# Kernel tuning notes

Hardware: AMD Instinct MI355X
Metric: run time of the kernel (lower is better)

Reference implementation:

```python
import jax, jax.numpy as jnp
import numpy as np

SMU_ALPHA = 0.25
SMU_MU = 1.0e6  # repo's act.SMU default: large mu -> smooth leaky-relu (max(x, alpha*x))

def smu(x):
    a = SMU_ALPHA
    return 0.5 * ((1.0 + a) * x + (1.0 - a) * x * jax.lax.erf(SMU_MU * (1.0 - a) * x))

def setup_inputs() -> dict:
    key = jax.random.key(0)
    ks = jax.random.split(key, 6)
    B, N, D = 8, 4096, 1024
    xavier = float(np.sqrt(6.0 / (D + D)))
    def lin_w(k):
        return jax.random.uniform(k, (D, D), jnp.float32, -xavier, xavier)
    return {
        "x": jax.random.normal(ks[0], (B, N, D), jnp.float32),
        "Wvr": lin_w(ks[1]), "bvr": jnp.zeros((D,), jnp.float32),
        "Wvi": lin_w(ks[2]), "bvi": jnp.zeros((D,), jnp.float32),
        "Wk": lin_w(ks[3]), "bk": jnp.zeros((D,), jnp.float32),
        "Wq": lin_w(ks[4]), "bq": jnp.zeros((D,), jnp.float32),
    }

def reference(x, Wvr, bvr, Wvi, bvi, Wk, bk, Wq, bq):
    # real input: real and imag branches both see x
    value_real = jnp.einsum('bnd,ed->bne', x, Wvr) + bvr
    value_imag = jnp.einsum('bnd,ed->bne', x, Wvi) + bvi
    # GLU: v_real * tanh(softplus(v_imag)); dropout disabled (p=0)
    value = value_real * jnp.tanh(jax.nn.softplus(value_imag))
    key_ = jnp.einsum('bnd,ed->bne', x, Wk) + bk
    query = jnp.einsum('bnd,ed->bne', x, Wq) + bq
    # L2 normalize along the sequence dim (dim=1)
    key_n = key_ / (jnp.linalg.norm(key_, axis=1, keepdims=True) + 1e-5)
    query_n = query / (jnp.linalg.norm(query, axis=1, keepdims=True) + 1e-5)
    feature_attn = smu(jnp.einsum('bnd,bne->bde', key_n, query_n))  # [B, D, D]
    return jnp.einsum('bnd,bde->bne', value, feature_attn)
```

## Files before the change

kernel.cpp:

```cpp
#include <hip/hip_runtime.h>
#include <math.h>

typedef __bf16 bf16x8 __attribute__((ext_vector_type(8)));
typedef float f32x4 __attribute__((ext_vector_type(4)));

#define MTOT 32768
#define DD   1024
#define NSEQ 4096
#define BB   8

__device__ __forceinline__ void async16(const void* gp, void* lp) {
  __builtin_amdgcn_global_load_lds(
      (__attribute__((address_space(1))) void*)(const_cast<void*>(gp)),
      (__attribute__((address_space(3))) void*)(lp), 16, 0, 0);
}

__device__ __forceinline__ unsigned short f2bf(float f) {
  union { float f; unsigned int u; } v; v.f = f;
  unsigned int r = v.u + 0x7fffu + ((v.u >> 16) & 1u);
  return (unsigned short)(r >> 16);
}
__device__ __forceinline__ float bf2f(unsigned short u) {
  union { unsigned int u; float f; } v; v.u = ((unsigned int)u) << 16; return v.f;
}

__device__ __forceinline__ unsigned lds_off(void* p) {
  return (unsigned)(unsigned long long)
      (__attribute__((address_space(3))) void*)p;
}
__device__ __forceinline__ bf16x8 dsr128(unsigned a) {
  bf16x8 r;
  asm volatile("ds_read_b128 %0, %1" : "=v"(r) : "v"(a));
  return r;
}

__global__ void cvt_bf16(const float* __restrict__ in, unsigned short* __restrict__ out, int n) {
  int i = (blockIdx.x * blockDim.x + threadIdx.x) * 8;
  if (i >= n) return;
  float4 a = *(const float4*)(in + i);
  float4 b = *(const float4*)(in + i + 4);
  ushort4 o0, o1;
  o0.x = f2bf(a.x); o0.y = f2bf(a.y); o0.z = f2bf(a.z); o0.w = f2bf(a.w);
  o1.x = f2bf(b.x); o1.y = f2bf(b.y); o1.z = f2bf(b.z); o1.w = f2bf(b.w);
  *(ushort4*)(out + i) = o0;
  *(ushort4*)(out + i + 4) = o1;
}

__global__ void cvt_w(const float* __restrict__ w0, const float* __restrict__ w1,
                      const float* __restrict__ w2, const float* __restrict__ w3,
                      unsigned short* __restrict__ out) {
  int z = blockIdx.y;
  const float* in = (z == 0) ? w0 : (z == 1) ? w1 : (z == 2) ? w2 : w3;
  int i = (blockIdx.x * blockDim.x + threadIdx.x) * 8;
  float4 a = *(const float4*)(in + i);
  float4 b = *(const float4*)(in + i + 4);
  ushort4 o0, o1;
  o0.x = f2bf(a.x); o0.y = f2bf(a.y); o0.z = f2bf(a.z); o0.w = f2bf(a.w);
  o1.x = f2bf(b.x); o1.y = f2bf(b.y); o1.z = f2bf(b.z); o1.w = f2bf(b.w);
  unsigned short* o = out + (size_t)z * DD * DD;
  *(ushort4*)(o + i) = o0;
  *(ushort4*)(o + i + 4) = o1;
}

template<int LDG>
__device__ __forceinline__ void stage_half(const unsigned short* __restrict__ g,
                                           int row0, int k0,
                                           unsigned short* lds, int tid) {
#pragma unroll
  for (int l = 0; l < 2; ++l) {
    int u = l * 512 + tid;
    int r = u >> 3;
    int sl = (u & 7) ^ (r & 7);
    async16(g + (size_t)(row0 + r) * LDG + k0 + sl * 8, (char*)lds + u * 16);
  }
}

__global__ __launch_bounds__(512, 2) void proj_all(
    const unsigned short* __restrict__ xb,
    const unsigned short* __restrict__ Wb,
    const float* __restrict__ bvr, const float* __restrict__ bvi,
    const float* __restrict__ bk,  const float* __restrict__ bq,
    unsigned short* __restrict__ oVr, unsigned short* __restrict__ oVi,
    unsigned short* __restrict__ Kt,  unsigned short* __restrict__ Qt,
    float* __restrict__ rnacc) {
  __shared__ __align__(16) unsigned short smem[65536];

  const int bx = blockIdx.x;
  const int swz = (bx & 7) * 64 + (bx >> 3);
  const int m0 = (swz >> 2) * 256;
  const int n0 = (swz & 3) * 256;
  const int z = blockIdx.z;
  const unsigned short* W = Wb + (size_t)z * DD * DD;
  const float* bias = (z == 0) ? bvr : (z == 1) ? bvi : (z == 2) ? bk : bq;

  const int tid = threadIdx.x;
  const int w = tid >> 6, lane = tid & 63;
  const int wr = w >> 2, wc = w & 3;
  const int lq = lane >> 4, lr = lane & 15;
  const int sx = lr & 7;
  const int arow0 = wr * 128 + lr;
  const int brow0 = wc * 64 + lr;

  f32x4 acc[8][4];
#pragma unroll
  for (int i = 0; i < 8; i++)
#pragma unroll
    for (int j = 0; j < 4; j++) acc[i][j] = (f32x4)(0.f);

  const int NT = 16;

  const unsigned sbase = lds_off(smem);
  const unsigned sw0 = (unsigned)((lq ^ sx) << 4);
  const unsigned sw1 = (unsigned)(((4 | lq) ^ sx) << 4);
  unsigned aA0 = sbase + arow0 * 128 + sw0;
  unsigned aA1 = sbase + arow0 * 128 + sw1;
  unsigned aB0 = sbase + 32768 + brow0 * 128 + sw0;
  unsigned aB1 = sbase + 32768 + brow0 * 128 + sw1;

  stage_half<1024>(xb, m0,       0,  smem,                     tid);
  stage_half<1024>(xb, m0 + 128, 0,  smem + 8192,              tid);
  stage_half<1024>(W,  n0,       0,  smem + 16384,             tid);
  stage_half<1024>(W,  n0 + 128, 0,  smem + 16384 + 8192,      tid);
  stage_half<1024>(W,  n0,       64, smem + 32768 + 16384,     tid);
  stage_half<1024>(W,  n0 + 128, 64, smem + 32768 + 16384 + 8192, tid);
  asm volatile("s_waitcnt vmcnt(4)" ::: "memory");
  __builtin_amdgcn_s_barrier();

  for (int t = 0; t < NT; ++t) {
    bf16x8 bfr[4][2];
#pragma unroll
    for (int q = 0; q < 4; ++q) {
      bf16x8 afq[2][2];
      if (q == 0) {
#pragma unroll
        for (int nj = 0; nj < 4; ++nj) {
          bfr[nj][0] = dsr128(aB0 + nj * 2048u);
          bfr[nj][1] = dsr128(aB1 + nj * 2048u);
        }
      }
#pragma unroll
      for (int mi = 0; mi < 2; ++mi) {
        afq[mi][0] = dsr128(aA0 + (2 * q + mi) * 2048u);
        afq[mi][1] = dsr128(aA1 + (2 * q + mi) * 2048u);
      }
      if (q == 0) {
        if (t + 1 < NT)
          stage_half<1024>(xb, m0, (t + 1) * 64, smem + ((t + 1) & 1) * 32768, tid);
      } else if (q == 1) {
        if (t + 1 < NT)
          stage_half<1024>(xb, m0 + 128, (t + 1) * 64, smem + ((t + 1) & 1) * 32768 + 8192, tid);
      } else if (q == 2) {
        if (t + 2 < NT)
          stage_half<1024>(W, n0, (t + 2) * 64, smem + (t & 1) * 32768 + 16384, tid);
      } else {
        if (t + 2 < NT)
          stage_half<1024>(W, n0 + 128, (t + 2) * 64, smem + (t & 1) * 32768 + 16384 + 8192, tid);
      }
      __builtin_amdgcn_s_barrier();
      asm volatile("s_waitcnt lgkmcnt(0)" ::: "memory");
      __builtin_amdgcn_sched_barrier(0);
      __builtin_amdgcn_s_setprio(1);
#pragma unroll
      for (int mi = 0; mi < 2; ++mi)
#pragma unroll
        for (int nj = 0; nj < 4; ++nj)
#pragma unroll
          for (int ks = 0; ks < 2; ++ks)
            acc[2 * q + mi][nj] = __builtin_amdgcn_mfma_f32_16x16x32_bf16(
                afq[mi][ks], bfr[nj][ks], acc[2 * q + mi][nj], 0, 0, 0);
      __builtin_amdgcn_s_setprio(0);
      __builtin_amdgcn_sched_barrier(0);
      if (q == 3) {
        if (t < NT - 2)       asm volatile("s_waitcnt vmcnt(4)" ::: "memory");
        else if (t == NT - 2) asm volatile("s_waitcnt vmcnt(0)" ::: "memory");
      }
      __builtin_amdgcn_s_barrier();
    }
    aA0 ^= 65536u; aA1 ^= 65536u; aB0 ^= 65536u; aB1 ^= 65536u;
  }

  if (z < 2) {
    unsigned short* out = (z == 0) ? oVr : oVi;
#pragma unroll
    for (int nj = 0; nj < 4; ++nj) {
      int col = n0 + wc * 64 + nj * 16 + lr;
      float bv = bias[col];
#pragma unroll
      for (int mrep = 0; mrep < 8; ++mrep) {
        int rowb = m0 + wr * 128 + mrep * 16 + lq * 4;
#pragma unroll
        for (int r = 0; r < 4; ++r)
          out[(size_t)(rowb + r) * DD + col] = f2bf(acc[mrep][nj][r] + bv);
      }
    }
  } else {
    unsigned short* outp = (z == 2) ? Kt : Qt;
    const int which = z - 2;
    const int b = m0 >> 12;
    const int nbase = m0 & 4095;
    float* racc = rnacc + which * (BB * DD) + b * DD;
    unsigned short* T = smem;
    const int SP2 = 264;
#pragma unroll
    for (int ch = 0; ch < 2; ++ch) {
      if ((wc >> 1) == ch) {
#pragma unroll
        for (int nj = 0; nj < 4; ++nj) {
          int cloc = (wc & 1) * 64 + nj * 16 + lr;
          float bv = bias[n0 + ch * 128 + cloc];
#pragma unroll
          for (int mrep = 0; mrep < 8; ++mrep) {
            int rowb = wr * 128 + mrep * 16 + lq * 4;
            ushort4 pk;
            pk.x = f2bf(acc[mrep][nj][0] + bv); pk.y = f2bf(acc[mrep][nj][1] + bv);
            pk.z = f2bf(acc[mrep][nj][2] + bv); pk.w = f2bf(acc[mrep][nj][3] + bv);
            *(ushort4*)(T + cloc * SP2 + rowb) = pk;
          }
        }
      }
      __syncthreads();
#pragma unroll
      for (int p = 0; p < 8; ++p) {
        int dl = p * 16 + (tid >> 5);
        int nc = (tid & 31) * 8;
        ushort4 v0 = *(const ushort4*)(T + dl * SP2 + nc);
        ushort4 v1 = *(const ushort4*)(T + dl * SP2 + nc + 4);
        int d = n0 + ch * 128 + dl;
        *(ushort4*)(outp + (size_t)(b * DD + d) * NSEQ + nbase + nc)     = v0;
        *(ushort4*)(outp + (size_t)(b * DD + d) * NSEQ + nbase + nc + 4) = v1;
        float s = bf2f(v0.x)*bf2f(v0.x) + bf2f(v0.y)*bf2f(v0.y) + bf2f(v0.z)*bf2f(v0.z) + bf2f(v0.w)*bf2f(v0.w)
                + bf2f(v1.x)*bf2f(v1.x) + bf2f(v1.y)*bf2f(v1.y) + bf2f(v1.z)*bf2f(v1.z) + bf2f(v1.w)*bf2f(v1.w);
#pragma unroll
        for (int off = 1; off < 32; off <<= 1) s += __shfl_xor(s, off, 32);
        if ((tid & 31) == 0) atomicAdd(&racc[d], s);
      }
      __syncthreads();
    }
  }
}

__global__ void finalize_rn(float* __restrict__ rn) {
  int i = blockIdx.x * blockDim.x + threadIdx.x;
  rn[i] = 1.f / (sqrtf(rn[i]) + 1e-5f);
}

__global__ void glu(unsigned short* __restrict__ V, const unsigned short* __restrict__ Vi, int n) {
  int i = (blockIdx.x * blockDim.x + threadIdx.x) * 8;
  if (i >= n) return;
  ushort4 r0 = *(const ushort4*)(V + i);
  ushort4 r1 = *(const ushort4*)(V + i + 4);
  ushort4 i0 = *(const ushort4*)(Vi + i);
  ushort4 i1 = *(const ushort4*)(Vi + i + 4);
  unsigned short vr[8] = {r0.x, r0.y, r0.z, r0.w, r1.x, r1.y, r1.z, r1.w};
  unsigned short vi[8] = {i0.x, i0.y, i0.z, i0.w, i1.x, i1.y, i1.z, i1.w};
  unsigned short o[8];
#pragma unroll
  for (int k = 0; k < 8; k++) {
    float a = bf2f(vr[k]), b = bf2f(vi[k]);
    float g;
    if (b > 10.f) g = 1.f;
    else { float t = __expf(b); float u = t * (t + 2.f); g = u / (u + 2.f); }
    o[k] = f2bf(a * g);
  }
  *(ushort4*)(V + i)     = make_ushort4(o[0], o[1], o[2], o[3]);
  *(ushort4*)(V + i + 4) = make_ushort4(o[4], o[5], o[6], o[7]);
}

__global__ __launch_bounds__(512, 2) void attn_gemm(
    const unsigned short* __restrict__ Qt, const unsigned short* __restrict__ Kt,
    const float* __restrict__ rn, unsigned short* __restrict__ fat) {
  __shared__ __align__(16) unsigned short smem[57344];

  const int b = blockIdx.z;
  const int d0 = blockIdx.x * 128;
  const int e0 = blockIdx.y * 256;
  const unsigned short* A  = Qt + (size_t)b * DD * NSEQ;
  const unsigned short* Bm = Kt + (size_t)b * DD * NSEQ;
  unsigned short* out = fat + (size_t)b * DD * DD;

  const int tid = threadIdx.x;
  const int w = tid >> 6, lane = tid & 63;
  const int wr = w >> 1, wc = w & 1;
  const int lq = lane >> 4, lr = lane & 15;
  const int sx = lr & 7;
  const int arow0 = wr * 64 + lr;
  const int brow0 = wc * 64 + lr;

  f32x4 acc[4][4];
#pragma unroll
  for (int i = 0; i < 4; i++)
#pragma unroll
    for (int j = 0; j < 4; j++) acc[i][j] = (f32x4)(0.f);

  const int NT = 64;

  const unsigned sbase = lds_off(smem);
  const unsigned sw0 = (unsigned)((lq ^ sx) << 4);
  const unsigned sw1 = (unsigned)(((4 | lq) ^ sx) << 4);
  unsigned aA0 = sbase + arow0 * 128 + sw0;
  unsigned aA1 = sbase + arow0 * 128 + sw1;
  unsigned aB0 = sbase + 32768 + brow0 * 128 + sw0;
  unsigned aB1 = sbase + 32768 + brow0 * 128 + sw1;

  stage_half<NSEQ>(A,  e0,       0,  smem,                 tid);
  stage_half<NSEQ>(A,  e0 + 128, 0,  smem + 8192,          tid);
  stage_half<NSEQ>(Bm, d0,       0,  smem + 16384,         tid);
  stage_half<NSEQ>(Bm, d0,       64, smem + 32768 + 16384, tid);
  asm volatile("s_waitcnt vmcnt(2)" ::: "memory");
  __builtin_amdgcn_s_barrier();

  for (int t = 0; t < NT; ++t) {
    bf16x8 bfr[4][2];
#pragma unroll
    for (int q = 0; q < 4; ++q) {
      bf16x8 afq[2];
      if (q == 0) {
#pragma unroll
        for (int nj = 0; nj < 4; ++nj) {
          bfr[nj][0] = dsr128(aB0 + nj * 2048u);
          bfr[nj][1] = dsr128(aB1 + nj * 2048u);
        }
      }
      afq[0] = dsr128(aA0 + q * 2048u);
      afq[1] = dsr128(aA1 + q * 2048u);
      if (q == 0) {
        if (t + 1 < NT)
          stage_half<NSEQ>(A, e0, (t + 1) * 64, smem + ((t + 1) & 1) * 32768, tid);
      } else if (q == 1) {
        if (t + 1 < NT)
          stage_half<NSEQ>(A, e0 + 128, (t + 1) * 64, smem + ((t + 1) & 1) * 32768 + 8192, tid);
      } else if (q == 2) {
        if (t + 2 < NT)
          stage_half<NSEQ>(Bm, d0, (t + 2) * 64, smem + (t & 1) * 32768 + 16384, tid);
      }
      __builtin_amdgcn_s_barrier();
      asm volatile("s_waitcnt lgkmcnt(0)" ::: "memory");
      __builtin_amdgcn_sched_barrier(0);
      __builtin_amdgcn_s_setprio(1);
#pragma unroll
      for (int nj = 0; nj < 4; ++nj)
#pragma unroll
        for (int ks = 0; ks < 2; ++ks)
          acc[q][nj] = __builtin_amdgcn_mfma_f32_16x16x32_bf16(
              afq[ks], bfr[nj][ks], acc[q][nj], 0, 0, 0);
      __builtin_amdgcn_s_setprio(0);
      __builtin_amdgcn_sched_barrier(0);
      if (q == 3) {
        if (t < NT - 2)       asm volatile("s_waitcnt vmcnt(2)" ::: "memory");
        else if (t == NT - 2) asm volatile("s_waitcnt vmcnt(0)" ::: "memory");
      }
      __builtin_amdgcn_s_barrier();
    }
    aA0 ^= 65536u; aA1 ^= 65536u; aB0 ^= 65536u; aB1 ^= 65536u;
  }

#pragma unroll
  for (int nj = 0; nj < 4; ++nj) {
    int col = d0 + wc * 64 + nj * 16 + lr;
    float rk = rn[b * DD + col];
#pragma unroll
    for (int mi = 0; mi < 4; ++mi) {
      int rowb = e0 + wr * 64 + mi * 16 + lq * 4;
#pragma unroll
      for (int r = 0; r < 4; ++r) {
        float rq = rn[BB * DD + b * DD + rowb + r];
        float c = acc[mi][nj][r] * rq * rk;
        c = (c > 0.f) ? c : 0.25f * c;
        out[(size_t)(rowb + r) * DD + col] = f2bf(c);
      }
    }
  }
}

__global__ __launch_bounds__(512, 2) void out_gemm(
    const unsigned short* __restrict__ V, const unsigned short* __restrict__ fat,
    float* __restrict__ out) {
  __shared__ __align__(16) unsigned short smem[65536];

  const int bx = blockIdx.x;
  const int swz = (bx & 7) * 64 + (bx >> 3);
  const int m0 = (swz >> 2) * 256;
  const int e0 = (swz & 3) * 256;
  const int b = m0 >> 12;
  const unsigned short* Bm = fat + (size_t)b * DD * DD;

  const int tid = threadIdx.x;
  const int w = tid >> 6, lane = tid & 63;
  const int wr = w >> 2, wc = w & 3;
  const int lq = lane >> 4, lr = lane & 15;
  const int sx = lr & 7;
  const int arow0 = wr * 128 + lr;
  const int brow0 = wc * 64 + lr;

  f32x4 acc[8][4];
#pragma unroll
  for (int i = 0; i < 8; i++)
#pragma unroll
    for (int j = 0; j < 4; j++) acc[i][j] = (f32x4)(0.f);

  const int NT = 16;

  const unsigned sbase = lds_off(smem);
  const unsigned sw0 = (unsigned)((lq ^ sx) << 4);
  const unsigned sw1 = (unsigned)(((4 | lq) ^ sx) << 4);
  unsigned aA0 = sbase + arow0 * 128 + sw0;
  unsigned aA1 = sbase + arow0 * 128 + sw1;
  unsigned aB0 = sbase + 32768 + brow0 * 128 + sw0;
  unsigned aB1 = sbase + 32768 + brow0 * 128 + sw1;

  stage_half<1024>(V,  m0,       0,  smem,                        tid);
  stage_half<1024>(V,  m0 + 128, 0,  smem + 8192,                 tid);
  stage_half<1024>(Bm, e0,       0,  smem + 16384,                tid);
  stage_half<1024>(Bm, e0 + 128, 0,  smem + 16384 + 8192,         tid);
  stage_half<1024>(Bm, e0,       64, smem + 32768 + 16384,        tid);
  stage_half<1024>(Bm, e0 + 128, 64, smem + 32768 + 16384 + 8192, tid);
  asm volatile("s_waitcnt vmcnt(4)" ::: "memory");
  __builtin_amdgcn_s_barrier();

  for (int t = 0; t < NT; ++t) {
    bf16x8 bfr[4][2];
#pragma unroll
    for (int q = 0; q < 4; ++q) {
      bf16x8 afq[2][2];
      if (q == 0) {
#pragma unroll
        for (int nj = 0; nj < 4; ++nj) {
          bfr[nj][0] = dsr128(aB0 + nj * 2048u);
          bfr[nj][1] = dsr128(aB1 + nj * 2048u);
        }
      }
#pragma unroll
      for (int mi = 0; mi < 2; ++mi) {
        afq[mi][0] = dsr128(aA0 + (2 * q + mi) * 2048u);
        afq[mi][1] = dsr128(aA1 + (2 * q + mi) * 2048u);
      }
      if (q == 0) {
        if (t + 1 < NT)
          stage_half<1024>(V, m0, (t + 1) * 64, smem + ((t + 1) & 1) * 32768, tid);
      } else if (q == 1) {
        if (t + 1 < NT)
          stage_half<1024>(V, m0 + 128, (t + 1) * 64, smem + ((t + 1) & 1) * 32768 + 8192, tid);
      } else if (q == 2) {
        if (t + 2 < NT)
          stage_half<1024>(Bm, e0, (t + 2) * 64, smem + (t & 1) * 32768 + 16384, tid);
      } else {
        if (t + 2 < NT)
          stage_half<1024>(Bm, e0 + 128, (t + 2) * 64, smem + (t & 1) * 32768 + 16384 + 8192, tid);
      }
      __builtin_amdgcn_s_barrier();
      asm volatile("s_waitcnt lgkmcnt(0)" ::: "memory");
      __builtin_amdgcn_sched_barrier(0);
      __builtin_amdgcn_s_setprio(1);
#pragma unroll
      for (int mi = 0; mi < 2; ++mi)
#pragma unroll
        for (int nj = 0; nj < 4; ++nj)
#pragma unroll
          for (int ks = 0; ks < 2; ++ks)
            acc[2 * q + mi][nj] = __builtin_amdgcn_mfma_f32_16x16x32_bf16(
                afq[mi][ks], bfr[nj][ks], acc[2 * q + mi][nj], 0, 0, 0);
      __builtin_amdgcn_s_setprio(0);
      __builtin_amdgcn_sched_barrier(0);
      if (q == 3) {
        if (t < NT - 2)       asm volatile("s_waitcnt vmcnt(4)" ::: "memory");
        else if (t == NT - 2) asm volatile("s_waitcnt vmcnt(0)" ::: "memory");
      }
      __builtin_amdgcn_s_barrier();
    }
    aA0 ^= 65536u; aA1 ^= 65536u; aB0 ^= 65536u; aB1 ^= 65536u;
  }

#pragma unroll
  for (int nj = 0; nj < 4; ++nj) {
    int col = e0 + wc * 64 + nj * 16 + lr;
#pragma unroll
    for (int mrep = 0; mrep < 8; ++mrep) {
      int rowb = m0 + wr * 128 + mrep * 16 + lq * 4;
#pragma unroll
      for (int r = 0; r < 4; ++r)
        out[(size_t)(rowb + r) * DD + col] = acc[mrep][nj][r];
    }
  }
}

extern "C" void kernel_launch(void* const* d_in, const int* in_sizes, int n_in,
                              void* d_out, int out_size, void* d_ws, size_t ws_size,
                              hipStream_t stream) {
  const float* x   = (const float*)d_in[0];
  const float* Wvr = (const float*)d_in[1];
  const float* bvr = (const float*)d_in[2];
  const float* Wvi = (const float*)d_in[3];
  const float* bvi = (const float*)d_in[4];
  const float* Wk  = (const float*)d_in[5];
  const float* bk  = (const float*)d_in[6];
  const float* Wq  = (const float*)d_in[7];
  const float* bq  = (const float*)d_in[8];
  float* out = (float*)d_out;

  char* p = (char*)d_ws;
  unsigned short* xb  = (unsigned short*)p; p += (size_t)MTOT * DD * 2;
  unsigned short* Wb  = (unsigned short*)p; p += 4ull * DD * DD * 2;
  unsigned short* Kt  = (unsigned short*)p; p += (size_t)BB * DD * NSEQ * 2;
  unsigned short* Qt  = (unsigned short*)p; p += (size_t)BB * DD * NSEQ * 2;
  unsigned short* Vb  = (unsigned short*)p; p += (size_t)MTOT * DD * 2;
  unsigned short* fat = (unsigned short*)p; p += (size_t)BB * DD * DD * 2;
  float* rn = (float*)p; p += 2ull * BB * DD * sizeof(float);

  unsigned short* ViBuf = (unsigned short*)d_out;

  int nx = MTOT * DD;
  int nw = DD * DD;
  cvt_bf16<<<nx / 8 / 256, 256, 0, stream>>>(x, xb, nx);
  cvt_w<<<dim3(nw / 8 / 256, 4), 256, 0, stream>>>(Wvr, Wvi, Wk, Wq, Wb);
  hipMemsetAsync(rn, 0, 2ull * BB * DD * sizeof(float), stream);

  proj_all<<<dim3(512, 1, 4), 512, 0, stream>>>(
      xb, Wb, bvr, bvi, bk, bq, Vb, ViBuf, Kt, Qt, rn);

  glu<<<nx / 8 / 256, 256, 0, stream>>>(Vb, ViBuf, nx);
  finalize_rn<<<2 * BB * DD / 256, 256, 0, stream>>>(rn);

  attn_gemm<<<dim3(DD / 128, DD / 256, BB), 512, 0, stream>>>(Qt, Kt, rn, fat);
  out_gemm<<<dim3(512), 512, 0, stream>>>(Vb, fat, out);
}
```

Baseline: 738.8 us.

## Restructure GEMM k-loops into two phases with partial LDS waits

Each of the three GEMM main loops goes from four sub-phases per k-tile, each with two barriers, to two phases. Each phase issues its LDS reads up front with immediate offsets instead of computed addresses, then waits only for the first fragments (partial lgkmcnt) before starting MFMAs. The remaining fragments arrive while the first MFMAs run. This halves the barrier count and overlaps LDS latency with compute, at the cost of more live fragment registers (aL/aH), which could raise VGPR pressure.

```diff
diff --git a/kernel.cpp b/kernel.cpp
--- a/kernel.cpp
+++ b/kernel.cpp
@@ -28,11 +28,10 @@
   return (unsigned)(unsigned long long)
       (__attribute__((address_space(3))) void*)p;
 }
-__device__ __forceinline__ bf16x8 dsr128(unsigned a) {
-  bf16x8 r;
-  asm volatile("ds_read_b128 %0, %1" : "=v"(r) : "v"(a));
-  return r;
-}
+#define DSRI(dst, base, off) \
+  asm volatile("ds_read_b128 %0, %1 offset:" #off : "=v"(dst) : "v"(base))
+
+#define MFMA_ __builtin_amdgcn_mfma_f32_16x16x32_bf16
 
 __global__ void cvt_bf16(const float* __restrict__ in, unsigned short* __restrict__ out, int n) {
   int i = (blockIdx.x * blockDim.x + threadIdx.x) * 8;
@@ -127,55 +126,76 @@
   __builtin_amdgcn_s_barrier();
 
   for (int t = 0; t < NT; ++t) {
-    bf16x8 bfr[4][2];
-#pragma unroll
-    for (int q = 0; q < 4; ++q) {
-      bf16x8 afq[2][2];
-      if (q == 0) {
-#pragma unroll
-        for (int nj = 0; nj < 4; ++nj) {
-          bfr[nj][0] = dsr128(aB0 + nj * 2048u);
-          bfr[nj][1] = dsr128(aB1 + nj * 2048u);
-        }
-      }
-#pragma unroll
-      for (int mi = 0; mi < 2; ++mi) {
-        afq[mi][0] = dsr128(aA0 + (2 * q + mi) * 2048u);
-        afq[mi][1] = dsr128(aA1 + (2 * q + mi) * 2048u);
-      }
-      if (q == 0) {
-        if (t + 1 < NT)
-          stage_half<1024>(xb, m0, (t + 1) * 64, smem + ((t + 1) & 1) * 32768, tid);
-      } else if (q == 1) {
-        if (t + 1 < NT)
-          stage_half<1024>(xb, m0 + 128, (t + 1) * 64, smem + ((t + 1) & 1) * 32768 + 8192, tid);
-      } else if (q == 2) {
-        if (t + 2 < NT)
-          stage_half<1024>(W, n0, (t + 2) * 64, smem + (t & 1) * 32768 + 16384, tid);
-      } else {
-        if (t + 2 < NT)
-          stage_half<1024>(W, n0 + 128, (t + 2) * 64, smem + (t & 1) * 32768 + 16384 + 8192, tid);
-      }
-      __builtin_amdgcn_s_barrier();
-      asm volatile("s_waitcnt lgkmcnt(0)" ::: "memory");
-      __builtin_amdgcn_sched_barrier(0);
-      __builtin_amdgcn_s_setprio(1);
-#pragma unroll
-      for (int mi = 0; mi < 2; ++mi)
-#pragma unroll
-        for (int nj = 0; nj < 4; ++nj)
-#pragma unroll
-          for (int ks = 0; ks < 2; ++ks)
-            acc[2 * q + mi][nj] = __builtin_amdgcn_mfma_f32_16x16x32_bf16(
-                afq[mi][ks], bfr[nj][ks], acc[2 * q + mi][nj], 0, 0, 0);
-      __builtin_amdgcn_s_setprio(0);
-      __builtin_amdgcn_sched_barrier(0);
-      if (q == 3) {
-        if (t < NT - 2)       asm volatile("s_waitcnt vmcnt(4)" ::: "memory");
-        else if (t == NT - 2) asm volatile("s_waitcnt vmcnt(0)" ::: "memory");
-      }
-      __builtin_amdgcn_s_barrier();
-    }
+    bf16x8 bfr[4][2], aL[4][2];
+    DSRI(aL[0][0], aA0, 0);    DSRI(aL[0][1], aA1, 0);
+    DSRI(bfr[0][0], aB0, 0);    DSRI(bfr[0][1], aB1, 0);
+    DSRI(bfr[1][0], aB0, 2048); DSRI(bfr[1][1], aB1, 2048);
+    DSRI(bfr[2][0], aB0, 4096); DSRI(bfr[2][1], aB1, 4096);
+    DSRI(bfr[3][0], aB0, 6144); DSRI(bfr[3][1], aB1, 6144);
+    DSRI(aL[1][0], aA0, 2048); DSRI(aL[1][1], aA1, 2048);
+    DSRI(aL[2][0], aA0, 4096); DSRI(aL[2][1], aA1, 4096);
+    DSRI(aL[3][0], aA0, 6144); DSRI(aL[3][1], aA1, 6144);
+    if (t + 1 < NT) {
+      stage_half<1024>(xb, m0,       (t + 1) * 64, smem + ((t + 1) & 1) * 32768, tid);
+      stage_half<1024>(xb, m0 + 128, (t + 1) * 64, smem + ((t + 1) & 1) * 32768 + 8192, tid);
+    }
+    __builtin_amdgcn_s_barrier();
+    asm volatile("s_waitcnt lgkmcnt(6)" ::: "memory");
+    __builtin_amdgcn_sched_barrier(0);
+    __builtin_amdgcn_s_setprio(1);
+#pragma unroll
+    for (int nj = 0; nj < 4; ++nj) {
+      acc[0][nj] = MFMA_(aL[0][0], bfr[nj][0], acc[0][nj], 0, 0, 0);
+      acc[0][nj] = MFMA_(aL[0][1], bfr[nj][1], acc[0][nj], 0, 0, 0);
+    }
+    asm volatile("s_waitcnt lgkmcnt(0)" ::: "memory");
+    __builtin_amdgcn_sched_barrier(0);
+#pragma unroll
+    for (int mi = 1; mi < 4; ++mi)
+#pragma unroll
+      for (int nj = 0; nj < 4; ++nj) {
+        acc[mi][nj] = MFMA_(aL[mi][0], bfr[nj][0], acc[mi][nj], 0, 0, 0);
+        acc[mi][nj] = MFMA_(aL[mi][1], bfr[nj][1], acc[mi][nj], 0, 0, 0);
+      }
+    __builtin_amdgcn_s_setprio(0);
+    __builtin_amdgcn_sched_barrier(0);
+    __builtin_amdgcn_s_barrier();
+
+    bf16x8 aH[4][2];
+    DSRI(aH[0][0], aA0, 8192);  DSRI(aH[0][1], aA1, 8192);
+    DSRI(aH[1][0], aA0, 10240); DSRI(aH[1][1], aA1, 10240);
+    DSRI(aH[2][0], aA0, 12288); DSRI(aH[2][1], aA1, 12288);
+    DSRI(aH[3][0], aA0, 14336); DSRI(aH[3][1], aA1, 14336);
+    if (t + 2 < NT) {
+      stage_half<1024>(W, n0,       (t + 2) * 64, smem + (t & 1) * 32768 + 16384, tid);
+      stage_half<1024>(W, n0 + 128, (t + 2) * 64, smem + (t & 1) * 32768 + 16384 + 8192, tid);
+    }
+    __builtin_amdgcn_s_barrier();
+    asm volatile("s_waitcnt lgkmcnt(4)" ::: "memory");
+    __builtin_amdgcn_sched_barrier(0);
+    __builtin_amdgcn_s_setprio(1);
+#pragma unroll
+    for (int mi = 0; mi < 2; ++mi)
+#pragma unroll
+      for (int nj = 0; nj < 4; ++nj) {
+        acc[4 + mi][nj] = MFMA_(aH[mi][0], bfr[nj][0], acc[4 + mi][nj], 0, 0, 0);
+        acc[4 + mi][nj] = MFMA_(aH[mi][1], bfr[nj][1], acc[4 + mi][nj], 0, 0, 0);
+      }
+    asm volatile("s_waitcnt lgkmcnt(0)" ::: "memory");
+    __builtin_amdgcn_sched_barrier(0);
+#pragma unroll
+    for (int mi = 2; mi < 4; ++mi)
+#pragma unroll
+      for (int nj = 0; nj < 4; ++nj) {
+        acc[4 + mi][nj] = MFMA_(aH[mi][0], bfr[nj][0], acc[4 + mi][nj], 0, 0, 0);
+        acc[4 + mi][nj] = MFMA_(aH[mi][1], bfr[nj][1], acc[4 + mi][nj], 0, 0, 0);
+      }
+    __builtin_amdgcn_s_setprio(0);
+    __builtin_amdgcn_sched_barrier(0);
+    if (t < NT - 2)       asm volatile("s_waitcnt vmcnt(4)" ::: "memory");
+    else if (t == NT - 2) asm volatile("s_waitcnt vmcnt(0)" ::: "memory");
+    __builtin_amdgcn_s_barrier();
+
     aA0 ^= 65536u; aA1 ^= 65536u; aB0 ^= 65536u; aB1 ^= 65536u;
   }
 
@@ -310,47 +330,65 @@
   __builtin_amdgcn_s_barrier();
 
   for (int t = 0; t < NT; ++t) {
-    bf16x8 bfr[4][2];
-#pragma unroll
-    for (int q = 0; q < 4; ++q) {
-      bf16x8 afq[2];
-      if (q == 0) {
-#pragma unroll
-        for (int nj = 0; nj < 4; ++nj) {
-          bfr[nj][0] = dsr128(aB0 + nj * 2048u);
-          bfr[nj][1] = dsr128(aB1 + nj * 2048u);
-        }
-      }
-      afq[0] = dsr128(aA0 + q * 2048u);
-      afq[1] = dsr128(aA1 + q * 2048u);
-      if (q == 0) {
-        if (t + 1 < NT)
-          stage_half<NSEQ>(A, e0, (t + 1) * 64, smem + ((t + 1) & 1) * 32768, tid);
-      } else if (q == 1) {
-        if (t + 1 < NT)
-          stage_half<NSEQ>(A, e0 + 128, (t + 1) * 64, smem + ((t + 1) & 1) * 32768 + 8192, tid);
-      } else if (q == 2) {
-        if (t + 2 < NT)
-          stage_half<NSEQ>(Bm, d0, (t + 2) * 64, smem + (t & 1) * 32768 + 16384, tid);
-      }
-      __builtin_amdgcn_s_barrier();
-      asm volatile("s_waitcnt lgkmcnt(0)" ::: "memory");
-      __builtin_amdgcn_sched_barrier(0);
-      __builtin_amdgcn_s_setprio(1);
-#pragma unroll
-      for (int nj = 0; nj < 4; ++nj)
-#pragma unroll
-        for (int ks = 0; ks < 2; ++ks)
-          acc[q][nj] = __builtin_amdgcn_mfma_f32_16x16x32_bf16(
-              afq[ks], bfr[nj][ks], acc[q][nj], 0, 0, 0);
-      __builtin_amdgcn_s_setprio(0);
-      __builtin_amdgcn_sched_barrier(0);
-      if (q == 3) {
-        if (t < NT - 2)       asm volatile("s_waitcnt vmcnt(2)" ::: "memory");
-        else if (t == NT - 2) asm volatile("s_waitcnt vmcnt(0)" ::: "memory");
-      }
-      __builtin_amdgcn_s_barrier();
-    }
+    bf16x8 bfr[4][2], aL[2][2];
+    DSRI(aL[0][0], aA0, 0);    DSRI(aL[0][1], aA1, 0);
+    DSRI(bfr[0][0], aB0, 0);    DSRI(bfr[0][1], aB1, 0);
+    DSRI(bfr[1][0], aB0, 2048); DSRI(bfr[1][1], aB1, 2048);
+    DSRI(bfr[2][0], aB0, 4096); DSRI(bfr[2][1], aB1, 4096);
+    DSRI(bfr[3][0], aB0, 6144); DSRI(bfr[3][1], aB1, 6144);
+    DSRI(aL[1][0], aA0, 2048); DSRI(aL[1][1], aA1, 2048);
+    if (t + 1 < NT) {
+      stage_half<NSEQ>(A, e0,       (t + 1) * 64, smem + ((t + 1) & 1) * 32768, tid);
+      stage_half<NSEQ>(A, e0 + 128, (t + 1) * 64, smem + ((t + 1) & 1) * 32768 + 8192, tid);
+    }
+    __builtin_amdgcn_s_barrier();
+    asm volatile("s_waitcnt lgkmcnt(2)" ::: "memory");
+    __builtin_amdgcn_sched_barrier(0);
+    __builtin_amdgcn_s_setprio(1);
+#pragma unroll
+    for (int nj = 0; nj < 4; ++nj) {
+      acc[0][nj] = MFMA_(aL[0][0], bfr[nj][0], acc[0][nj], 0, 0, 0);
+      acc[0][nj] = MFMA_(aL[0][1], bfr[nj][1], acc[0][nj], 0, 0, 0);
+    }
+    asm volatile("s_waitcnt lgkmcnt(0)" ::: "memory");
+    __builtin_amdgcn_sched_barrier(0);
+#pragma unroll
+    for (int nj = 0; nj < 4; ++nj) {
+      acc[1][nj] = MFMA_(aL[1][0], bfr[nj][0], acc[1][nj], 0, 0, 0);
+      acc[1][nj] = MFMA_(aL[1][1], bfr[nj][1], acc[1][nj], 0, 0, 0);
+    }
+    __builtin_amdgcn_s_setprio(0);
+    __builtin_amdgcn_sched_barrier(0);
+    __builtin_amdgcn_s_barrier();
+
+    bf16x8 aH[2][2];
+    DSRI(aH[0][0], aA0, 4096); DSRI(aH[0][1], aA1, 4096);
+    DSRI(aH[1][0], aA0, 6144); DSRI(aH[1][1], aA1, 6144);
+    if (t + 2 < NT) {
+      stage_half<NSEQ>(Bm, d0, (t + 2) * 64, smem + (t & 1) * 32768 + 16384, tid);
+    }
+    __builtin_amdgcn_s_barrier();
+    asm volatile("s_waitcnt lgkmcnt(2)" ::: "memory");
+    __builtin_amdgcn_sched_barrier(0);
+    __builtin_amdgcn_s_setprio(1);
+#pragma unroll
+    for (int nj = 0; nj < 4; ++nj) {
+      acc[2][nj] = MFMA_(aH[0][0], bfr[nj][0], acc[2][nj], 0, 0, 0);
+      acc[2][nj] = MFMA_(aH[0][1], bfr[nj][1], acc[2][nj], 0, 0, 0);
+    }
+    asm volatile("s_waitcnt lgkmcnt(0)" ::: "memory");
+    __builtin_amdgcn_sched_barrier(0);
+#pragma unroll
+    for (int nj = 0; nj < 4; ++nj) {
+      acc[3][nj] = MFMA_(aH[1][0], bfr[nj][0], acc[3][nj], 0, 0, 0);
+      acc[3][nj] = MFMA_(aH[1][1], bfr[nj][1], acc[3][nj], 0, 0, 0);
+    }
+    __builtin_amdgcn_s_setprio(0);
+    __builtin_amdgcn_sched_barrier(0);
+    if (t < NT - 2)       asm volatile("s_waitcnt vmcnt(2)" ::: "memory");
+    else if (t == NT - 2) asm volatile("s_waitcnt vmcnt(0)" ::: "memory");
+    __builtin_amdgcn_s_barrier();
+
     aA0 ^= 65536u; aA1 ^= 65536u; aB0 ^= 65536u; aB1 ^= 65536u;
   }
 
@@ -418,55 +456,76 @@
   __builtin_amdgcn_s_barrier();
 
   for (int t = 0; t < NT; ++t) {
-    bf16x8 bfr[4][2];
-#pragma unroll
-    for (int q = 0; q < 4; ++q) {
-      bf16x8 afq[2][2];
-      if (q == 0) {
-#pragma unroll
-        for (int nj = 0; nj < 4; ++nj) {
-          bfr[nj][0] = dsr128(aB0 + nj * 2048u);
-          bfr[nj][1] = dsr128(aB1 + nj * 2048u);
-        }
-      }
-#pragma unroll
-      for (int mi = 0; mi < 2; ++mi) {
-        afq[mi][0] = dsr128(aA0 + (2 * q + mi) * 2048u);
-        afq[mi][1] = dsr128(aA1 + (2 * q + mi) * 2048u);
-      }
-      if (q == 0) {
-        if (t + 1 < NT)
-          stage_half<1024>(V, m0, (t + 1) * 64, smem + ((t + 1) & 1) * 32768, tid);
-      } else if (q == 1) {
-        if (t + 1 < NT)
-          stage_half<1024>(V, m0 + 128, (t + 1) * 64, smem + ((t + 1) & 1) * 32768 + 8192, tid);
-      } else if (q == 2) {
-        if (t + 2 < NT)
-          stage_half<1024>(Bm, e0, (t + 2) * 64, smem + (t & 1) * 32768 + 16384, tid);
-      } else {
-        if (t + 2 < NT)
-          stage_half<1024>(Bm, e0 + 128, (t + 2) * 64, smem + (t & 1) * 32768 + 16384 + 8192, tid);
-      }
-      __builtin_amdgcn_s_barrier();
-      asm volatile("s_waitcnt lgkmcnt(0)" ::: "memory");
-      __builtin_amdgcn_sched_barrier(0);
-      __builtin_amdgcn_s_setprio(1);
-#pragma unroll
-      for (int mi = 0; mi < 2; ++mi)
-#pragma unroll
-        for (int nj = 0; nj < 4; ++nj)
-#pragma unroll
-          for (int ks = 0; ks < 2; ++ks)
-            acc[2 * q + mi][nj] = __builtin_amdgcn_mfma_f32_16x16x32_bf16(
-                afq[mi][ks], bfr[nj][ks], acc[2 * q + mi][nj], 0, 0, 0);
-      __builtin_amdgcn_s_setprio(0);
-      __builtin_amdgcn_sched_barrier(0);
-      if (q == 3) {
-        if (t < NT - 2)       asm volatile("s_waitcnt vmcnt(4)" ::: "memory");
-        else if (t == NT - 2) asm volatile("s_waitcnt vmcnt(0)" ::: "memory");
-      }
-      __builtin_amdgcn_s_barrier();
-    }
+    bf16x8 bfr[4][2], aL[4][2];
+    DSRI(aL[0][0], aA0, 0);    DSRI(aL[0][1], aA1, 0);
+    DSRI(bfr[0][0], aB0, 0);    DSRI(bfr[0][1], aB1, 0);
+    DSRI(bfr[1][0], aB0, 2048); DSRI(bfr[1][1], aB1, 2048);
+    DSRI(bfr[2][0], aB0, 4096); DSRI(bfr[2][1], aB1, 4096);
+    DSRI(bfr[3][0], aB0, 6144); DSRI(bfr[3][1], aB1, 6144);
+    DSRI(aL[1][0], aA0, 2048); DSRI(aL[1][1], aA1, 2048);
+    DSRI(aL[2][0], aA0, 4096); DSRI(aL[2][1], aA1, 4096);
+    DSRI(aL[3][0], aA0, 6144); DSRI(aL[3][1], aA1, 6144);
+    if (t + 1 < NT) {
+      stage_half<1024>(V, m0,       (t + 1) * 64, smem + ((t + 1) & 1) * 32768, tid);
+      stage_half<1024>(V, m0 + 128, (t + 1) * 64, smem + ((t + 1) & 1) * 32768 + 8192, tid);
+    }
+    __builtin_amdgcn_s_barrier();
+    asm volatile("s_waitcnt lgkmcnt(6)" ::: "memory");
+    __builtin_amdgcn_sched_barrier(0);
+    __builtin_amdgcn_s_setprio(1);
+#pragma unroll
+    for (int nj = 0; nj < 4; ++nj) {
+      acc[0][nj] = MFMA_(aL[0][0], bfr[nj][0], acc[0][nj], 0, 0, 0);
+      acc[0][nj] = MFMA_(aL[0][1], bfr[nj][1], acc[0][nj], 0, 0, 0);
+    }
+    asm volatile("s_waitcnt lgkmcnt(0)" ::: "memory");
+    __builtin_amdgcn_sched_barrier(0);
+#pragma unroll
+    for (int mi = 1; mi < 4; ++mi)
+#pragma unroll
+      for (int nj = 0; nj < 4; ++nj) {
+        acc[mi][nj] = MFMA_(aL[mi][0], bfr[nj][0], acc[mi][nj], 0, 0, 0);
+        acc[mi][nj] = MFMA_(aL[mi][1], bfr[nj][1], acc[mi][nj], 0, 0, 0);
+      }
+    __builtin_amdgcn_s_setprio(0);
+    __builtin_amdgcn_sched_barrier(0);
+    __builtin_amdgcn_s_barrier();
+
+    bf16x8 aH[4][2];
+    DSRI(aH[0][0], aA0, 8192);  DSRI(aH[0][1], aA1, 8192);
+    DSRI(aH[1][0], aA0, 10240); DSRI(aH[1][1], aA1, 10240);
+    DSRI(aH[2][0], aA0, 12288); DSRI(aH[2][1], aA1, 12288);
+    DSRI(aH[3][0], aA0, 14336); DSRI(aH[3][1], aA1, 14336);
+    if (t + 2 < NT) {
+      stage_half<1024>(Bm, e0,       (t + 2) * 64, smem + (t & 1) * 32768 + 16384, tid);
+      stage_half<1024>(Bm, e0 + 128, (t + 2) * 64, smem + (t & 1) * 32768 + 16384 + 8192, tid);
+    }
+    __builtin_amdgcn_s_barrier();
+    asm volatile("s_waitcnt lgkmcnt(4)" ::: "memory");
+    __builtin_amdgcn_sched_barrier(0);
+    __builtin_amdgcn_s_setprio(1);
+#pragma unroll
+    for (int mi = 0; mi < 2; ++mi)
+#pragma unroll
+      for (int nj = 0; nj < 4; ++nj) {
+        acc[4 + mi][nj] = MFMA_(aH[mi][0], bfr[nj][0], acc[4 + mi][nj], 0, 0, 0);
+        acc[4 + mi][nj] = MFMA_(aH[mi][1], bfr[nj][1], acc[4 + mi][nj], 0, 0, 0);
+      }
+    asm volatile("s_waitcnt lgkmcnt(0)" ::: "memory");
+    __builtin_amdgcn_sched_barrier(0);
+#pragma unroll
+    for (int mi = 2; mi < 4; ++mi)
+#pragma unroll
+      for (int nj = 0; nj < 4; ++nj) {
+        acc[4 + mi][nj] = MFMA_(aH[mi][0], bfr[nj][0], acc[4 + mi][nj], 0, 0, 0);
+        acc[4 + mi][nj] = MFMA_(aH[mi][1], bfr[nj][1], acc[4 + mi][nj], 0, 0, 0);
+      }
+    __builtin_amdgcn_s_setprio(0);
+    __builtin_amdgcn_sched_barrier(0);
+    if (t < NT - 2)       asm volatile("s_waitcnt vmcnt(4)" ::: "memory");
+    else if (t == NT - 2) asm volatile("s_waitcnt vmcnt(0)" ::: "memory");
+    __builtin_amdgcn_s_barrier();
+
     aA0 ^= 65536u; aA1 ^= 65536u; aB0 ^= 65536u; aB1 ^= 65536u;
   }
 
```

Result: no change. 729.9 us (-1.2%).
